# Optimization experiments

Measured on AMD Instinct MI355X. Metric: run time of the kernel, lower is better.

## Reference

```python
import jax, jax.numpy as jnp
import numpy as np

D_MODEL = 1024
N_INPUT = 4096
N_PROCESS = 2048
D_ROUTING = 256
TEMPERATURE = 0.5
LN_EPS = 1e-5


def _gelu(x):
    return jax.nn.gelu(x, approximate=False)  # torch F.gelu default (erf)


def setup_inputs() -> dict:
    key = jax.random.key(0)
    ks = jax.random.split(key, 10)
    B, S = 8, 2048
    x = jax.random.normal(ks[0], (B, S, D_MODEL), dtype=jnp.float32)
    # GlobalRouter query_net: Linear(d_model, 2*d_routing) -> GELU -> LayerNorm -> Linear(2*d_routing, d_routing)
    W1 = jax.random.normal(ks[1], (2 * D_ROUTING, D_MODEL), dtype=jnp.float32) * (2.0 / (D_MODEL + 2 * D_ROUTING)) ** 0.5 * 1.414
    b1 = jnp.zeros((2 * D_ROUTING,), dtype=jnp.float32)
    ln_g = jnp.ones((2 * D_ROUTING,), dtype=jnp.float32)
    ln_b = jnp.zeros((2 * D_ROUTING,), dtype=jnp.float32)
    W2 = jax.random.normal(ks[2], (D_ROUTING, 2 * D_ROUTING), dtype=jnp.float32) * (2.0 / (3 * D_ROUTING)) ** 0.5 * 1.414
    b2 = jnp.zeros((D_ROUTING,), dtype=jnp.float32)
    neuron_keys = jax.random.normal(ks[3], (N_INPUT, D_ROUTING), dtype=jnp.float32) / D_ROUTING ** 0.5 * 1.414
    input_patterns = jax.random.normal(ks[4], (N_INPUT, D_MODEL), dtype=jnp.float32) / D_MODEL ** 0.5 * 1.414
    process_weights = jax.random.normal(ks[5], (N_PROCESS, N_INPUT), dtype=jnp.float32) / N_INPUT ** 0.5 * 1.414
    process_outputs = jax.random.normal(ks[6], (N_PROCESS, D_MODEL), dtype=jnp.float32) / D_MODEL ** 0.5 * 1.414
    return {
        'x': x, 'k_input': 2048, 'k_process': 1024,
        'W1': W1, 'b1': b1, 'ln_g': ln_g, 'ln_b': ln_b, 'W2': W2, 'b2': b2,
        'neuron_keys': neuron_keys, 'input_patterns': input_patterns,
        'process_weights': process_weights, 'process_outputs': process_outputs,
    }


def _forward(x, k_input, k_process, W1, b1, ln_g, ln_b, W2, b2,
             neuron_keys, input_patterns, process_weights, process_outputs):
    B, S, d_model = x.shape
    # ---- GlobalRouter ----
    gctx = jnp.max(x, axis=1)                                  # [B, d_model]
    h = _gelu(gctx @ W1.T + b1)                                # [B, 2*d_routing]
    mu = jnp.mean(h, axis=-1, keepdims=True)
    var = jnp.mean((h - mu) ** 2, axis=-1, keepdims=True)
    h = (h - mu) * jax.lax.rsqrt(var + LN_EPS) * ln_g + ln_b
    query = h @ W2.T + b2                                      # [B, d_routing]
    logits = (query @ neuron_keys.T) / D_ROUTING ** 0.5        # [B, n_input]
    probs = jax.nn.softmax(logits / TEMPERATURE, axis=-1)
    _, input_idx = jax.lax.top_k(logits, k_input)              # [B, k_input]
    one_hot = jnp.zeros_like(probs).at[jnp.arange(B)[:, None], input_idx].set(1.0)
    routing_weights = jax.lax.stop_gradient(one_hot - probs) + probs  # STE
    # ---- input neuron stage ----
    input_acts = _gelu(jnp.einsum('bsd,nd->bsn', x, input_patterns))   # [B,S,n_input]
    weighted = input_acts * routing_weights[:, None, :]
    sel_in = jnp.take_along_axis(weighted, input_idx[:, None, :], axis=2)  # [B,S,k_input]
    # gather process weight columns per batch: [B, n_process, k_input]
    W_sel = jnp.transpose(process_weights[:, input_idx], (1, 0, 2))
    process_acts = _gelu(jnp.einsum('bsk,bpk->bsp', sel_in, W_sel))    # [B,S,n_process]
    # ---- process neuron stage ----
    process_scores = jnp.mean(process_acts, axis=1)                    # [B,n_process]
    _, process_idx = jax.lax.top_k(process_scores, k_process)          # [B,k_process]
    sel_proc = jnp.take_along_axis(process_acts, process_idx[:, None, :], axis=2)  # [B,S,k_process]
    out_sel = process_outputs[process_idx]                             # [B,k_process,d_model]
    return jnp.einsum('bsp,bpd->bsd', sel_proc, out_sel)


def reference(x, k_input, k_process, W1, b1, ln_g, ln_b, W2, b2,
              neuron_keys, input_patterns, process_weights, process_outputs):
    return _forward(x, k_input, k_process, W1, b1, ln_g, ln_b, W2, b2,
                    neuron_keys, input_patterns, process_weights, process_outputs)
```

## Files before the change

kernel.cpp:

```cpp
#include <hip/hip_runtime.h>
#include <stdint.h>

#define B_  8
#define S_  2048
#define DM  1024
#define NI  4096
#define NP  2048
#define DR  256
#define H2  512
#define KI  2048
#define KP  1024
#define LDW 40

typedef __attribute__((ext_vector_type(8))) short bf16x8;
typedef __attribute__((ext_vector_type(4))) float f32x4;
typedef unsigned short ushort;
typedef unsigned int uint;

__device__ __forceinline__ float gelu_erf(float v){
    return 0.5f * v * (1.0f + erff(v * 0.7071067811865476f));
}
__device__ __forceinline__ ushort f2b(float f){
    union { float f; uint u; } a; a.f = f;
    uint r = a.u + 0x7fffu + ((a.u >> 16) & 1u);
    return (ushort)(r >> 16);
}
__device__ __forceinline__ float b2f(ushort u){
    union { uint u; float f; } a; a.u = ((uint)u) << 16; return a.f;
}
__device__ __forceinline__ void cvt8(const float* p, uint4& H, uint4& L){
    uint h[4], l[4];
    #pragma unroll
    for(int i = 0; i < 4; i++){
        ushort h0 = f2b(p[2*i]);   float f0 = b2f(h0); ushort l0 = f2b(p[2*i]   - f0);
        ushort h1 = f2b(p[2*i+1]); float f1 = b2f(h1); ushort l1 = f2b(p[2*i+1] - f1);
        h[i] = (uint)h0 | ((uint)h1 << 16);
        l[i] = (uint)l0 | ((uint)l1 << 16);
    }
    H = uint4{h[0],h[1],h[2],h[3]};
    L = uint4{l[0],l[1],l[2],l[3]};
}
__device__ __forceinline__ void gload_lds16(const void* g, void* l){
    __builtin_amdgcn_global_load_lds((const __attribute__((address_space(1))) void*)g,
                                     (__attribute__((address_space(3))) void*)l, 16, 0, 0);
}

__global__ __launch_bounds__(256) void k_cvt(const float* __restrict__ src,
                                             ushort* __restrict__ hi,
                                             ushort* __restrict__ lo){
    size_t idx = (size_t)blockIdx.x*256 + threadIdx.x;
    float f[8];
    *(float4*)(f)     = ((const float4*)src)[idx*2];
    *(float4*)(f + 4) = ((const float4*)src)[idx*2 + 1];
    uint4 H, L; cvt8(f, H, L);
    ((uint4*)hi)[idx] = H;
    ((uint4*)lo)[idx] = L;
}

__global__ __launch_bounds__(256) void k_gpart(const float* __restrict__ x,
                                               float* __restrict__ gpart){
    int b = blockIdx.x >> 4, ch = blockIdx.x & 15;
    const float4* xb = (const float4*)(x + ((size_t)b*S_ + (size_t)ch*128) * DM);
    int t = threadIdx.x;
    float4 m = xb[t];
    for(int r = 1; r < 128; r++){
        float4 v = xb[(size_t)r*(DM/4) + t];
        m.x = fmaxf(m.x, v.x); m.y = fmaxf(m.y, v.y);
        m.z = fmaxf(m.z, v.z); m.w = fmaxf(m.w, v.w);
    }
    ((float4*)(gpart + (size_t)(b*16 + ch)*DM))[t] = m;
}

__global__ __launch_bounds__(256) void k_h(const float* __restrict__ gpart,
                                           const float* __restrict__ W1,
                                           const float* __restrict__ b1,
                                           float* __restrict__ h){
    __shared__ float g[DM];
    int b = blockIdx.x >> 3, ig = blockIdx.x & 7;
    int t = threadIdx.x;
    for(int d = t; d < DM; d += 256){
        float m = gpart[(size_t)(b*16)*DM + d];
        for(int c = 1; c < 16; c++) m = fmaxf(m, gpart[(size_t)(b*16 + c)*DM + d]);
        g[d] = m;
    }
    __syncthreads();
    int i  = ig*64 + (t >> 2);
    int dq = (t & 3) * 256;
    const float* wr = W1 + (size_t)i*DM + dq;
    const float* gg = g + dq;
    float s = 0.f;
    for(int d = 0; d < 256; d++) s = fmaf(gg[d], wr[d], s);
    s += __shfl_xor(s, 1);
    s += __shfl_xor(s, 2);
    if((t & 3) == 0) h[b*H2 + i] = gelu_erf(s + b1[i]);
}

__global__ __launch_bounds__(256) void k_query(const float* __restrict__ h,
                                               const float* __restrict__ lng,
                                               const float* __restrict__ lnb,
                                               const float* __restrict__ W2,
                                               const float* __restrict__ b2,
                                               float* __restrict__ query){
    __shared__ float hn[H2];
    __shared__ float red[4];
    int b = blockIdx.x >> 2, qg = blockIdx.x & 3;
    int t = threadIdx.x;
    float v0 = h[b*H2 + t], v1 = h[b*H2 + 256 + t];
    float s = v0 + v1;
    for(int o = 32; o > 0; o >>= 1) s += __shfl_down(s, o);
    if((t & 63) == 0) red[t >> 6] = s;
    __syncthreads();
    float mean = (red[0] + red[1] + red[2] + red[3]) * (1.f/H2);
    __syncthreads();
    float d0 = v0 - mean, d1 = v1 - mean;
    float sq = d0*d0 + d1*d1;
    for(int o = 32; o > 0; o >>= 1) sq += __shfl_down(sq, o);
    if((t & 63) == 0) red[t >> 6] = sq;
    __syncthreads();
    float var  = (red[0] + red[1] + red[2] + red[3]) * (1.f/H2);
    float rstd = rsqrtf(var + 1e-5f);
    hn[t]       = d0*rstd*lng[t]       + lnb[t];
    hn[256 + t] = d1*rstd*lng[256 + t] + lnb[256 + t];
    __syncthreads();
    int q  = qg*64 + (t >> 2);
    int iq = (t & 3) * 128;
    const float* wr = W2 + (size_t)q*H2 + iq;
    float acc = 0.f;
    for(int i2 = 0; i2 < 128; i2++) acc = fmaf(hn[iq + i2], wr[i2], acc);
    acc += __shfl_xor(acc, 1);
    acc += __shfl_xor(acc, 2);
    if((t & 3) == 0) query[b*DR + q] = acc + b2[q];
}

__global__ __launch_bounds__(256) void k_logits(const float* __restrict__ query,
                                                const float* __restrict__ nk,
                                                float* __restrict__ logits){
    __shared__ float q[DR];
    int b = blockIdx.x >> 4, ng = blockIdx.x & 15;
    int t = threadIdx.x;
    if(t < DR) q[t] = query[b*DR + t];
    __syncthreads();
    int n = ng*256 + t;
    const float* kr = nk + (size_t)n*DR;
    float s = 0.f;
    for(int i = 0; i < DR; i++) s = fmaf(q[i], kr[i], s);
    logits[b*NI + n] = s * 0.0625f;
}

template<int N_, int KSEL>
__global__ __launch_bounds__(256) void k_topk(const float* __restrict__ vals,
                                              int* __restrict__ idxout){
    __shared__ unsigned u[N_];
    __shared__ int redc[4];
    __shared__ int sc[256];
    int t = threadIdx.x;
    size_t vbase = (size_t)blockIdx.x * N_;
    size_t obase = (size_t)blockIdx.x * KSEL;
    for(int i = t; i < N_; i += 256){
        unsigned bits = __float_as_uint(vals[vbase + i]);
        u[i] = (bits & 0x80000000u) ? ~bits : (bits | 0x80000000u);
    }
    __syncthreads();
    unsigned lo = 0u, hi = 0xFFFFFFFFu;
    while(lo < hi){
        unsigned mid = lo + (unsigned)((((unsigned long long)(hi - lo)) + 1ull) >> 1);
        int c = 0;
        for(int i = t; i < N_; i += 256) c += (u[i] >= mid) ? 1 : 0;
        for(int o = 32; o > 0; o >>= 1) c += __shfl_down(c, o);
        if((t & 63) == 0) redc[t >> 6] = c;
        __syncthreads();
        int tot = redc[0] + redc[1] + redc[2] + redc[3];
        if(tot >= KSEL) lo = mid; else hi = mid - 1;
        __syncthreads();
    }
    unsigned T = lo;
    const int PER = N_ / 256;
    int base = t * PER;
    int lgt = 0, leq = 0;
    for(int j = 0; j < PER; j++){
        unsigned v = u[base + j];
        lgt += (v > T) ? 1 : 0; leq += (v == T) ? 1 : 0;
    }
    sc[t] = (lgt << 16) | leq;
    __syncthreads();
    for(int o = 1; o < 256; o <<= 1){
        int add = (t >= o) ? sc[t - o] : 0;
        __syncthreads();
        sc[t] += add;
        __syncthreads();
    }
    int need = KSEL - (sc[255] >> 16);
    int ex = (t == 0) ? 0 : sc[t - 1];
    int pos = (ex >> 16) + ((ex & 0xffff) < need ? (ex & 0xffff) : need);
    int eq = ex & 0xffff;
    for(int j = 0; j < PER; j++){
        unsigned v = u[base + j];
        if(v > T){ idxout[obase + pos++] = base + j; }
        else if(v == T){ if(eq < need){ idxout[obase + pos++] = base + j; } eq++; }
    }
}

__global__ __launch_bounds__(256) void k_gemm1(const ushort* __restrict__ xh,
                                               const ushort* __restrict__ xl,
                                               const ushort* __restrict__ ph,
                                               const ushort* __restrict__ pl,
                                               const int* __restrict__ iidx,
                                               ushort* __restrict__ selh,
                                               ushort* __restrict__ sell, int b0){
    __shared__ __align__(16) ushort Ah[2][128*32], Al[2][128*32], Bh[2][128*32], Bl[2][128*32];
    __shared__ int rowmap[128];
    int t = threadIdx.x;
    int g = blockIdx.x >> 8, rest = blockIdx.x & 255;
    int b = b0 + g;
    int mb = rest >> 4, nb = rest & 15;
    int m0 = mb*128, n0 = nb*128;
    ushort* selh_g = selh + (size_t)g*S_*KI;
    ushort* sell_g = sell + (size_t)g*S_*KI;
    if(t < 128) rowmap[t] = iidx[(size_t)b*KI + n0 + t];
    __syncthreads();
    int w = t >> 6, l = t & 63;
    int lr = l >> 2, lc = l & 3;
    int r0 = 32*w + lr, r1 = r0 + 16;
    const ushort* pAh0 = xh + ((size_t)b*S_ + m0 + r0)*DM + lc*8;
    const ushort* pAh1 = xh + ((size_t)b*S_ + m0 + r1)*DM + lc*8;
    const ushort* pAl0 = xl + ((size_t)b*S_ + m0 + r0)*DM + lc*8;
    const ushort* pAl1 = xl + ((size_t)b*S_ + m0 + r1)*DM + lc*8;
    const ushort* pBh0 = ph + (size_t)rowmap[r0]*DM + lc*8;
    const ushort* pBh1 = ph + (size_t)rowmap[r1]*DM + lc*8;
    const ushort* pBl0 = pl + (size_t)rowmap[r0]*DM + lc*8;
    const ushort* pBl1 = pl + (size_t)rowmap[r1]*DM + lc*8;
    int d0 = w*1024, d1 = d0 + 512;
    #define STG1(BUF, KO) do{ \
        gload_lds16(pAh0 + (KO), &Ah[BUF][d0]); \
        gload_lds16(pAh1 + (KO), &Ah[BUF][d1]); \
        gload_lds16(pAl0 + (KO), &Al[BUF][d0]); \
        gload_lds16(pAl1 + (KO), &Al[BUF][d1]); \
        gload_lds16(pBh0 + (KO), &Bh[BUF][d0]); \
        gload_lds16(pBh1 + (KO), &Bh[BUF][d1]); \
        gload_lds16(pBl0 + (KO), &Bl[BUF][d0]); \
        gload_lds16(pBl1 + (KO), &Bl[BUF][d1]); \
    }while(0)
    STG1(0, 0);
    int lm = l & 15, q = l >> 4;
    int mbase = (w >> 1)*64, nbase = (w & 1)*64;
    f32x4 acc[4][4];
    #pragma unroll
    for(int i = 0; i < 4; i++)
      #pragma unroll
      for(int j = 0; j < 4; j++) acc[i][j] = f32x4{0.f,0.f,0.f,0.f};
    int cur = 0;
    for(int k0 = 0; k0 < DM; k0 += 32){
        if(k0 + 32 < DM){
            STG1(cur^1, k0 + 32);
            asm volatile("s_waitcnt vmcnt(8)" ::: "memory");
        }else{
            asm volatile("s_waitcnt vmcnt(0)" ::: "memory");
        }
        __builtin_amdgcn_s_barrier();
        asm volatile("" ::: "memory");
        bf16x8 ahf[4], alf[4];
        #pragma unroll
        for(int mt = 0; mt < 4; mt++){
            ahf[mt] = *(const bf16x8*)(&Ah[cur][(mbase + mt*16 + lm)*32 + q*8]);
            alf[mt] = *(const bf16x8*)(&Al[cur][(mbase + mt*16 + lm)*32 + q*8]);
        }
        __builtin_amdgcn_s_setprio(1);
        #pragma unroll
        for(int nt = 0; nt < 4; nt++){
            bf16x8 bhf = *(const bf16x8*)(&Bh[cur][(nbase + nt*16 + lm)*32 + q*8]);
            bf16x8 blf = *(const bf16x8*)(&Bl[cur][(nbase + nt*16 + lm)*32 + q*8]);
            #pragma unroll
            for(int mt = 0; mt < 4; mt++){
                acc[mt][nt] = __builtin_amdgcn_mfma_f32_16x16x32_bf16(ahf[mt], bhf, acc[mt][nt], 0, 0, 0);
                acc[mt][nt] = __builtin_amdgcn_mfma_f32_16x16x32_bf16(ahf[mt], blf, acc[mt][nt], 0, 0, 0);
                acc[mt][nt] = __builtin_amdgcn_mfma_f32_16x16x32_bf16(alf[mt], bhf, acc[mt][nt], 0, 0, 0);
            }
        }
        __builtin_amdgcn_s_setprio(0);
        asm volatile("s_waitcnt lgkmcnt(0)" ::: "memory");
        __builtin_amdgcn_s_barrier();
        asm volatile("" ::: "memory");
        cur ^= 1;
    }
    #undef STG1
    #pragma unroll
    for(int mt = 0; mt < 4; mt++)
      #pragma unroll
      for(int nt = 0; nt < 4; nt++){
        int col = n0 + nbase + nt*16 + lm;
        #pragma unroll
        for(int i = 0; i < 4; i++){
            int row = m0 + mbase + mt*16 + q*4 + i;
            float gv = gelu_erf(acc[mt][nt][i]);
            ushort hbits = f2b(gv);
            selh_g[(size_t)row*KI + col] = hbits;
            sell_g[(size_t)row*KI + col] = f2b(gv - b2f(hbits));
        }
      }
}

__global__ __launch_bounds__(256) void k_gather_wsel(const float* __restrict__ pw,
                                                     const int* __restrict__ iidx,
                                                     ushort* __restrict__ wh,
                                                     ushort* __restrict__ wl,
                                                     float* __restrict__ scores, int b0){
    __shared__ int kidx[KI];
    int g = blockIdx.x >> 8, pc = blockIdx.x & 255;
    int b = b0 + g;
    ushort* wh_g = wh + (size_t)g*NP*KI;
    ushort* wl_g = wl + (size_t)g*NP*KI;
    int t = threadIdx.x;
    for(int i = t; i < KI; i += 256) kidx[i] = iidx[(size_t)b*KI + i];
    if(t < 8) scores[(size_t)b*NP + pc*8 + t] = 0.f;
    __syncthreads();
    for(int r2 = 0; r2 < 8; r2++){
        int p = pc*8 + r2;
        const float* row = pw + (size_t)p*NI;
        for(int j = t; j < KI; j += 256){
            float v = row[kidx[j]];
            ushort hb = f2b(v);
            wh_g[(size_t)p*KI + j] = hb;
            wl_g[(size_t)p*KI + j] = f2b(v - b2f(hb));
        }
    }
}

__global__ __launch_bounds__(256) void k_gemm2(const ushort* __restrict__ selh,
                                               const ushort* __restrict__ sell,
                                               const ushort* __restrict__ wh,
                                               const ushort* __restrict__ wl,
                                               ushort* __restrict__ acts,
                                               float* __restrict__ scores, int b0){
    __shared__ __align__(16) ushort Ah[2][128*32], Al[2][128*32], Bh[2][128*32], Bl[2][128*32];
    __shared__ float colsum[128];
    int t = threadIdx.x;
    int g = blockIdx.x >> 8, rest = blockIdx.x & 255;
    int b = b0 + g;
    int mb = rest >> 4, nb = rest & 15;
    int m0 = mb*128, n0 = nb*128;
    const ushort* selh_g = selh + (size_t)g*S_*KI;
    const ushort* sell_g = sell + (size_t)g*S_*KI;
    const ushort* wh_g   = wh   + (size_t)g*NP*KI;
    const ushort* wl_g   = wl   + (size_t)g*NP*KI;
    ushort* acts_g = acts + (size_t)g*S_*NP;
    int w = t >> 6, l = t & 63;
    int lr = l >> 2, lc = l & 3;
    int r0 = 32*w + lr, r1 = r0 + 16;
    const ushort* pAh0 = selh_g + (size_t)(m0 + r0)*KI + lc*8;
    const ushort* pAh1 = selh_g + (size_t)(m0 + r1)*KI + lc*8;
    const ushort* pAl0 = sell_g + (size_t)(m0 + r0)*KI + lc*8;
    const ushort* pAl1 = sell_g + (size_t)(m0 + r1)*KI + lc*8;
    const ushort* pBh0 = wh_g + (size_t)(n0 + r0)*KI + lc*8;
    const ushort* pBh1 = wh_g + (size_t)(n0 + r1)*KI + lc*8;
    const ushort* pBl0 = wl_g + (size_t)(n0 + r0)*KI + lc*8;
    const ushort* pBl1 = wl_g + (size_t)(n0 + r1)*KI + lc*8;
    int d0 = w*1024, d1 = d0 + 512;
    #define STG2(BUF, KO) do{ \
        gload_lds16(pAh0 + (KO), &Ah[BUF][d0]); \
        gload_lds16(pAh1 + (KO), &Ah[BUF][d1]); \
        gload_lds16(pAl0 + (KO), &Al[BUF][d0]); \
        gload_lds16(pAl1 + (KO), &Al[BUF][d1]); \
        gload_lds16(pBh0 + (KO), &Bh[BUF][d0]); \
        gload_lds16(pBh1 + (KO), &Bh[BUF][d1]); \
        gload_lds16(pBl0 + (KO), &Bl[BUF][d0]); \
        gload_lds16(pBl1 + (KO), &Bl[BUF][d1]); \
    }while(0)
    STG2(0, 0);
    int lm = l & 15, q = l >> 4;
    int mbase = (w >> 1)*64, nbase = (w & 1)*64;
    f32x4 acc[4][4];
    #pragma unroll
    for(int i = 0; i < 4; i++)
      #pragma unroll
      for(int j = 0; j < 4; j++) acc[i][j] = f32x4{0.f,0.f,0.f,0.f};
    int cur = 0;
    for(int k0 = 0; k0 < KI; k0 += 32){
        if(k0 + 32 < KI){
            STG2(cur^1, k0 + 32);
            asm volatile("s_waitcnt vmcnt(8)" ::: "memory");
        }else{
            asm volatile("s_waitcnt vmcnt(0)" ::: "memory");
        }
        __builtin_amdgcn_s_barrier();
        asm volatile("" ::: "memory");
        bf16x8 ahf[4], alf[4];
        #pragma unroll
        for(int mt = 0; mt < 4; mt++){
            ahf[mt] = *(const bf16x8*)(&Ah[cur][(mbase + mt*16 + lm)*32 + q*8]);
            alf[mt] = *(const bf16x8*)(&Al[cur][(mbase + mt*16 + lm)*32 + q*8]);
        }
        __builtin_amdgcn_s_setprio(1);
        #pragma unroll
        for(int nt = 0; nt < 4; nt++){
            bf16x8 bhf = *(const bf16x8*)(&Bh[cur][(nbase + nt*16 + lm)*32 + q*8]);
            bf16x8 blf = *(const bf16x8*)(&Bl[cur][(nbase + nt*16 + lm)*32 + q*8]);
            #pragma unroll
            for(int mt = 0; mt < 4; mt++){
                acc[mt][nt] = __builtin_amdgcn_mfma_f32_16x16x32_bf16(ahf[mt], bhf, acc[mt][nt], 0, 0, 0);
                acc[mt][nt] = __builtin_amdgcn_mfma_f32_16x16x32_bf16(ahf[mt], blf, acc[mt][nt], 0, 0, 0);
                acc[mt][nt] = __builtin_amdgcn_mfma_f32_16x16x32_bf16(alf[mt], bhf, acc[mt][nt], 0, 0, 0);
            }
        }
        __builtin_amdgcn_s_setprio(0);
        asm volatile("s_waitcnt lgkmcnt(0)" ::: "memory");
        __builtin_amdgcn_s_barrier();
        asm volatile("" ::: "memory");
        cur ^= 1;
    }
    #undef STG2
    if(t < 128) colsum[t] = 0.f;
    __syncthreads();
    #pragma unroll
    for(int mt = 0; mt < 4; mt++)
      #pragma unroll
      for(int nt = 0; nt < 4; nt++){
        int cb = nbase + nt*16 + lm;
        float s4 = 0.f;
        #pragma unroll
        for(int i = 0; i < 4; i++){
            int row = m0 + mbase + mt*16 + q*4 + i;
            float gv = gelu_erf(acc[mt][nt][i]);
            s4 += gv;
            acts_g[(size_t)row*NP + n0 + cb] = f2b(gv);
        }
        atomicAdd(&colsum[cb], s4);
      }
    __syncthreads();
    if(t < 128) atomicAdd(&scores[(size_t)b*NP + n0 + t], colsum[t]);
}

__global__ __launch_bounds__(256) void k_gather_selacts(const ushort* __restrict__ acts,
                                                        const int* __restrict__ pidx,
                                                        ushort* __restrict__ selacts, int b0){
    __shared__ int pix[KP];
    int g = blockIdx.x >> 6, sc_ = blockIdx.x & 63;
    int b = b0 + g;
    const ushort* acts_g = acts + (size_t)g*S_*NP;
    ushort* selacts_g = selacts + (size_t)g*S_*KP;
    int t = threadIdx.x;
    for(int i = t; i < KP; i += 256) pix[i] = pidx[(size_t)b*KP + i];
    __syncthreads();
    const ushort* Ab = acts_g    + ((size_t)sc_*32)*NP;
    ushort*       Ob = selacts_g + ((size_t)sc_*32)*KP;
    for(int r2 = 0; r2 < 32; r2++){
        for(int j = t; j < KP; j += 256)
            Ob[(size_t)r2*KP + j] = Ab[(size_t)r2*NP + pix[j]];
    }
}

__global__ __launch_bounds__(256) void k_gemm3(const ushort* __restrict__ selacts,
                                               const float* __restrict__ pout,
                                               const int* __restrict__ pidx,
                                               float* __restrict__ out, int b0){
    __shared__ __align__(16) ushort As[128*LDW], Bs[128*LDW];
    __shared__ int pix[KP];
    int t = threadIdx.x;
    int g = blockIdx.x >> 7, rest = blockIdx.x & 127;
    int b = b0 + g;
    int mb = rest >> 3, nb = rest & 7;
    int m0 = mb*128, n0 = nb*128;
    const ushort* selacts_g = selacts + (size_t)g*S_*KP;
    for(int i = t; i < KP; i += 256) pix[i] = pidx[(size_t)b*KP + i];
    __syncthreads();
    int r = t & 127, half = t >> 7;
    const ushort* ag = selacts_g + (size_t)(m0 + r)*KP + half*16;
    int kk = t >> 3, nc = (t & 7)*16;
    uint4 A0 = *(const uint4*)(ag), A1 = *(const uint4*)(ag + 8);
    float4 fb[4];
    {
        const float* bg = pout + (size_t)pix[kk]*DM + n0 + nc;
        #pragma unroll
        for(int i = 0; i < 4; i++) fb[i] = *(const float4*)(bg + i*4);
    }
    int w = t >> 6, lane = t & 63;
    int mbase = (w >> 1)*64, nbase = (w & 1)*64;
    int lm = lane & 15, q = lane >> 4;
    f32x4 acc[4][4];
    #pragma unroll
    for(int i = 0; i < 4; i++)
      #pragma unroll
      for(int j = 0; j < 4; j++) acc[i][j] = f32x4{0.f,0.f,0.f,0.f};
    for(int k0 = 0; k0 < KP; k0 += 32){
        __syncthreads();
        *(uint4*)(As + r*LDW + half*16)     = A0;
        *(uint4*)(As + r*LDW + half*16 + 8) = A1;
        {
            const float* pf = (const float*)fb;
            #pragma unroll
            for(int c = 0; c < 16; c++) Bs[(nc + c)*LDW + kk] = f2b(pf[c]);
        }
        __syncthreads();
        if(k0 + 32 < KP){
            ag += 32;
            A0 = *(const uint4*)(ag); A1 = *(const uint4*)(ag + 8);
            const float* bg = pout + (size_t)pix[k0 + 32 + kk]*DM + n0 + nc;
            #pragma unroll
            for(int i = 0; i < 4; i++) fb[i] = *(const float4*)(bg + i*4);
        }
        bf16x8 af[4];
        #pragma unroll
        for(int mt = 0; mt < 4; mt++)
            af[mt] = *(const bf16x8*)(As + (mbase + mt*16 + lm)*LDW + q*8);
        #pragma unroll
        for(int nt = 0; nt < 4; nt++){
            bf16x8 bf = *(const bf16x8*)(Bs + (nbase + nt*16 + lm)*LDW + q*8);
            #pragma unroll
            for(int mt = 0; mt < 4; mt++)
                acc[mt][nt] = __builtin_amdgcn_mfma_f32_16x16x32_bf16(af[mt], bf, acc[mt][nt], 0, 0, 0);
        }
    }
    float* Cb = out + (size_t)b*S_*DM;
    #pragma unroll
    for(int mt = 0; mt < 4; mt++)
      #pragma unroll
      for(int nt = 0; nt < 4; nt++){
        int col = n0 + nbase + nt*16 + lm;
        #pragma unroll
        for(int i = 0; i < 4; i++){
            int row = m0 + mbase + mt*16 + q*4 + i;
            Cb[(size_t)row*DM + col] = acc[mt][nt][i];
        }
      }
}

extern "C" void kernel_launch(void* const* d_in, const int* in_sizes, int n_in,
                              void* d_out, int out_size, void* d_ws, size_t ws_size,
                              hipStream_t stream){
    const float* x    = (const float*)d_in[0];
    const float* W1   = (const float*)d_in[3];
    const float* b1   = (const float*)d_in[4];
    const float* lng  = (const float*)d_in[5];
    const float* lnb  = (const float*)d_in[6];
    const float* W2   = (const float*)d_in[7];
    const float* b2   = (const float*)d_in[8];
    const float* nk   = (const float*)d_in[9];
    const float* patt = (const float*)d_in[10];
    const float* pw   = (const float*)d_in[11];
    const float* pout = (const float*)d_in[12];
    float* out = (float*)d_out;

    auto al256 = [](size_t v){ return (v + 255) & ~(size_t)255; };
    const size_t fixed =
        al256((size_t)B_*16*DM*4) + al256((size_t)B_*H2*4) + al256((size_t)B_*DR*4) +
        al256((size_t)B_*NI*4)    + al256((size_t)B_*KI*4) + al256((size_t)B_*NP*4) +
        al256((size_t)B_*KP*4) +
        2*al256((size_t)B_*S_*DM*2) + 2*al256((size_t)NI*DM*2);
    const size_t perb = (size_t)S_*KI*2*2 + (size_t)NP*KI*2*2 + (size_t)S_*NP*2 + (size_t)S_*KP*2 + 6*256;
    int G = 4;
    while(G > 1 && fixed + (size_t)G*perb > ws_size) G >>= 1;
    if(fixed + (size_t)G*perb > ws_size) return;

    char* wsp = (char*)d_ws;
    size_t off = 0;
    auto alloc = [&](size_t bytes) -> void* {
        void* p = wsp + off;
        off += (bytes + 255) & ~(size_t)255;
        return p;
    };
    float*  gpart   = (float*) alloc((size_t)B_*16*DM*4);
    float*  h       = (float*) alloc((size_t)B_*H2*4);
    float*  query   = (float*) alloc((size_t)B_*DR*4);
    float*  logits  = (float*) alloc((size_t)B_*NI*4);
    int*    iidx    = (int*)   alloc((size_t)B_*KI*4);
    float*  scores  = (float*) alloc((size_t)B_*NP*4);
    int*    pidx    = (int*)   alloc((size_t)B_*KP*4);
    ushort* xh      = (ushort*)alloc((size_t)B_*S_*DM*2);
    ushort* xl      = (ushort*)alloc((size_t)B_*S_*DM*2);
    ushort* patth   = (ushort*)alloc((size_t)NI*DM*2);
    ushort* pattl   = (ushort*)alloc((size_t)NI*DM*2);
    ushort* selh    = (ushort*)alloc((size_t)G*S_*KI*2);
    ushort* sell    = (ushort*)alloc((size_t)G*S_*KI*2);
    ushort* wselh   = (ushort*)alloc((size_t)G*NP*KI*2);
    ushort* wsell   = (ushort*)alloc((size_t)G*NP*KI*2);
    ushort* acts    = (ushort*)alloc((size_t)G*S_*NP*2);
    ushort* selacts = (ushort*)alloc((size_t)G*S_*KP*2);

    dim3 blk(256);
    k_cvt   <<<(B_*S_*DM/8)/256, blk, 0, stream>>>(x, xh, xl);
    k_cvt   <<<(NI*DM/8)/256,    blk, 0, stream>>>(patt, patth, pattl);
    k_gpart <<<128, blk, 0, stream>>>(x, gpart);
    k_h     <<<64,  blk, 0, stream>>>(gpart, W1, b1, h);
    k_query <<<32,  blk, 0, stream>>>(h, lng, lnb, W2, b2, query);
    k_logits<<<128, blk, 0, stream>>>(query, nk, logits);
    k_topk<NI, KI><<<B_, blk, 0, stream>>>(logits, iidx);
    for(int b0 = 0; b0 < B_; b0 += G){
        k_gemm1        <<<G*256, blk, 0, stream>>>(xh, xl, patth, pattl, iidx, selh, sell, b0);
        k_gather_wsel  <<<G*256, blk, 0, stream>>>(pw, iidx, wselh, wsell, scores, b0);
        k_gemm2        <<<G*256, blk, 0, stream>>>(selh, sell, wselh, wsell, acts, scores, b0);
        k_topk<NP, KP> <<<G,     blk, 0, stream>>>(scores + (size_t)b0*NP, pidx + (size_t)b0*KP);
        k_gather_selacts<<<G*64, blk, 0, stream>>>(acts, pidx, selacts, b0);
        k_gemm3        <<<G*128, blk, 0, stream>>>(selacts, pout, pidx, out, b0);
    }
}
```

Baseline: 1.465 ms.

## Fuse max-pool with x conversion, vectorize gathers, pipeline gemm3 with bf16 outputs

The global max over x is now computed in the same pass that converts x to bf16 hi/lo halves, so x is read once instead of twice. process_outputs is converted to bf16 once up front, and gemm3 double-buffers its A tile through direct global-to-LDS loads with explicit waitcnt and barriers. The index gathers in gather_wsel and gather_selacts read their indices straight into registers and issue vectorized stores. The default batch group size rises from 4 to 8 when workspace allows, cutting the number of loop iterations and launches. The cost is more workspace and hand-written synchronization in gemm3.

```diff
diff --git a/kernel.cpp b/kernel.cpp
--- a/kernel.cpp
+++ b/kernel.cpp
@@ -45,6 +45,29 @@
                                      (__attribute__((address_space(3))) void*)l, 16, 0, 0);
 }
 
+__global__ __launch_bounds__(256) void k_gpart_cvt(const float* __restrict__ x,
+                                                   float* __restrict__ gpart,
+                                                   ushort* __restrict__ xh,
+                                                   ushort* __restrict__ xl){
+    int b = blockIdx.x >> 5, ch = blockIdx.x & 31;
+    size_t row0 = (size_t)b*S_ + (size_t)ch*64;
+    const float4* xb = (const float4*)(x + row0*DM);
+    int t = threadIdx.x;
+    float4 m = float4{-3.402823466e38f, -3.402823466e38f, -3.402823466e38f, -3.402823466e38f};
+    for(int r = 0; r < 64; r++){
+        float4 v = xb[(size_t)r*(DM/4) + t];
+        ushort hx = f2b(v.x), hy = f2b(v.y), hz = f2b(v.z), hw = f2b(v.w);
+        uint2 H{ (uint)hx | ((uint)hy << 16), (uint)hz | ((uint)hw << 16) };
+        uint2 L{ (uint)f2b(v.x - b2f(hx)) | ((uint)f2b(v.y - b2f(hy)) << 16),
+                 (uint)f2b(v.z - b2f(hz)) | ((uint)f2b(v.w - b2f(hw)) << 16) };
+        ((uint2*)(xh + (row0 + r)*DM))[t] = H;
+        ((uint2*)(xl + (row0 + r)*DM))[t] = L;
+        m.x = fmaxf(m.x, v.x); m.y = fmaxf(m.y, v.y);
+        m.z = fmaxf(m.z, v.z); m.w = fmaxf(m.w, v.w);
+    }
+    ((float4*)(gpart + (size_t)(b*32 + ch)*DM))[t] = m;
+}
+
 __global__ __launch_bounds__(256) void k_cvt(const float* __restrict__ src,
                                              ushort* __restrict__ hi,
                                              ushort* __restrict__ lo){
@@ -57,18 +80,17 @@
     ((uint4*)lo)[idx] = L;
 }
 
-__global__ __launch_bounds__(256) void k_gpart(const float* __restrict__ x,
-                                               float* __restrict__ gpart){
-    int b = blockIdx.x >> 4, ch = blockIdx.x & 15;
-    const float4* xb = (const float4*)(x + ((size_t)b*S_ + (size_t)ch*128) * DM);
-    int t = threadIdx.x;
-    float4 m = xb[t];
-    for(int r = 1; r < 128; r++){
-        float4 v = xb[(size_t)r*(DM/4) + t];
-        m.x = fmaxf(m.x, v.x); m.y = fmaxf(m.y, v.y);
-        m.z = fmaxf(m.z, v.z); m.w = fmaxf(m.w, v.w);
-    }
-    ((float4*)(gpart + (size_t)(b*16 + ch)*DM))[t] = m;
+__global__ __launch_bounds__(256) void k_cvt1(const float* __restrict__ src,
+                                              ushort* __restrict__ dst){
+    size_t idx = (size_t)blockIdx.x*256 + threadIdx.x;
+    float f[8];
+    *(float4*)(f)     = ((const float4*)src)[idx*2];
+    *(float4*)(f + 4) = ((const float4*)src)[idx*2 + 1];
+    uint o[4];
+    #pragma unroll
+    for(int i = 0; i < 4; i++)
+        o[i] = (uint)f2b(f[2*i]) | ((uint)f2b(f[2*i+1]) << 16);
+    ((uint4*)dst)[idx] = uint4{o[0], o[1], o[2], o[3]};
 }
 
 __global__ __launch_bounds__(256) void k_h(const float* __restrict__ gpart,
@@ -79,8 +101,8 @@
     int b = blockIdx.x >> 3, ig = blockIdx.x & 7;
     int t = threadIdx.x;
     for(int d = t; d < DM; d += 256){
-        float m = gpart[(size_t)(b*16)*DM + d];
-        for(int c = 1; c < 16; c++) m = fmaxf(m, gpart[(size_t)(b*16 + c)*DM + d]);
+        float m = gpart[(size_t)(b*32)*DM + d];
+        for(int c = 1; c < 32; c++) m = fmaxf(m, gpart[(size_t)(b*32 + c)*DM + d]);
         g[d] = m;
     }
     __syncthreads();
@@ -304,24 +326,29 @@
                                                      ushort* __restrict__ wh,
                                                      ushort* __restrict__ wl,
                                                      float* __restrict__ scores, int b0){
-    __shared__ int kidx[KI];
     int g = blockIdx.x >> 8, pc = blockIdx.x & 255;
     int b = b0 + g;
     ushort* wh_g = wh + (size_t)g*NP*KI;
     ushort* wl_g = wl + (size_t)g*NP*KI;
     int t = threadIdx.x;
-    for(int i = t; i < KI; i += 256) kidx[i] = iidx[(size_t)b*KI + i];
     if(t < 8) scores[(size_t)b*NP + pc*8 + t] = 0.f;
-    __syncthreads();
+    int j0 = t*8;
+    int k8[8];
+    *(int4*)(k8)     = *(const int4*)(iidx + (size_t)b*KI + j0);
+    *(int4*)(k8 + 4) = *(const int4*)(iidx + (size_t)b*KI + j0 + 4);
     for(int r2 = 0; r2 < 8; r2++){
         int p = pc*8 + r2;
         const float* row = pw + (size_t)p*NI;
-        for(int j = t; j < KI; j += 256){
-            float v = row[kidx[j]];
-            ushort hb = f2b(v);
-            wh_g[(size_t)p*KI + j] = hb;
-            wl_g[(size_t)p*KI + j] = f2b(v - b2f(hb));
-        }
+        uint hh[4], ll[4];
+        #pragma unroll
+        for(int i = 0; i < 4; i++){
+            float v0 = row[k8[2*i]], v1 = row[k8[2*i+1]];
+            ushort h0 = f2b(v0), h1 = f2b(v1);
+            hh[i] = (uint)h0 | ((uint)h1 << 16);
+            ll[i] = (uint)f2b(v0 - b2f(h0)) | ((uint)f2b(v1 - b2f(h1)) << 16);
+        }
+        *(uint4*)(wh_g + (size_t)p*KI + j0) = uint4{hh[0],hh[1],hh[2],hh[3]};
+        *(uint4*)(wl_g + (size_t)p*KI + j0) = uint4{ll[0],ll[1],ll[2],ll[3]};
     }
 }
 
@@ -432,82 +459,99 @@
 __global__ __launch_bounds__(256) void k_gather_selacts(const ushort* __restrict__ acts,
                                                         const int* __restrict__ pidx,
                                                         ushort* __restrict__ selacts, int b0){
-    __shared__ int pix[KP];
     int g = blockIdx.x >> 6, sc_ = blockIdx.x & 63;
     int b = b0 + g;
     const ushort* acts_g = acts + (size_t)g*S_*NP;
     ushort* selacts_g = selacts + (size_t)g*S_*KP;
     int t = threadIdx.x;
-    for(int i = t; i < KP; i += 256) pix[i] = pidx[(size_t)b*KP + i];
-    __syncthreads();
+    int j0 = t*4;
+    int4 p4 = *(const int4*)(pidx + (size_t)b*KP + j0);
     const ushort* Ab = acts_g    + ((size_t)sc_*32)*NP;
     ushort*       Ob = selacts_g + ((size_t)sc_*32)*KP;
     for(int r2 = 0; r2 < 32; r2++){
-        for(int j = t; j < KP; j += 256)
-            Ob[(size_t)r2*KP + j] = Ab[(size_t)r2*NP + pix[j]];
+        const ushort* Ar = Ab + (size_t)r2*NP;
+        ushort o0 = Ar[p4.x], o1 = Ar[p4.y], o2 = Ar[p4.z], o3 = Ar[p4.w];
+        uint2 ov{ (uint)o0 | ((uint)o1 << 16), (uint)o2 | ((uint)o3 << 16) };
+        *(uint2*)(Ob + (size_t)r2*KP + j0) = ov;
     }
 }
 
 __global__ __launch_bounds__(256) void k_gemm3(const ushort* __restrict__ selacts,
-                                               const float* __restrict__ pout,
+                                               const ushort* __restrict__ poutb,
                                                const int* __restrict__ pidx,
                                                float* __restrict__ out, int b0){
-    __shared__ __align__(16) ushort As[128*LDW], Bs[128*LDW];
+    __shared__ __align__(16) ushort As[2][128*32];
+    __shared__ __align__(16) ushort Bs[2][128*LDW];
     __shared__ int pix[KP];
     int t = threadIdx.x;
     int g = blockIdx.x >> 7, rest = blockIdx.x & 127;
     int b = b0 + g;
     int mb = rest >> 3, nb = rest & 7;
     int m0 = mb*128, n0 = nb*128;
-    const ushort* selacts_g = selacts + (size_t)g*S_*KP;
+    const ushort* sel_g = selacts + (size_t)g*S_*KP;
+    int w = t >> 6, l = t & 63;
+    int lr = l >> 2, lc = l & 3;
+    int r0 = 32*w + lr, r1 = r0 + 16;
+    const ushort* pA0 = sel_g + (size_t)(m0 + r0)*KP + lc*8;
+    const ushort* pA1 = sel_g + (size_t)(m0 + r1)*KP + lc*8;
+    int d0 = w*1024, d1 = d0 + 512;
+    gload_lds16(pA0, &As[0][d0]);
+    gload_lds16(pA1, &As[0][d1]);
     for(int i = t; i < KP; i += 256) pix[i] = pidx[(size_t)b*KP + i];
     __syncthreads();
-    int r = t & 127, half = t >> 7;
-    const ushort* ag = selacts_g + (size_t)(m0 + r)*KP + half*16;
     int kk = t >> 3, nc = (t & 7)*16;
-    uint4 A0 = *(const uint4*)(ag), A1 = *(const uint4*)(ag + 8);
-    float4 fb[4];
+    uint4 B0, B1;
     {
-        const float* bg = pout + (size_t)pix[kk]*DM + n0 + nc;
-        #pragma unroll
-        for(int i = 0; i < 4; i++) fb[i] = *(const float4*)(bg + i*4);
-    }
-    int w = t >> 6, lane = t & 63;
+        const ushort* bg = poutb + (size_t)pix[kk]*DM + n0 + nc;
+        B0 = *(const uint4*)(bg); B1 = *(const uint4*)(bg + 8);
+    }
+    int lm = l & 15, q = l >> 4;
     int mbase = (w >> 1)*64, nbase = (w & 1)*64;
-    int lm = lane & 15, q = lane >> 4;
     f32x4 acc[4][4];
     #pragma unroll
     for(int i = 0; i < 4; i++)
       #pragma unroll
       for(int j = 0; j < 4; j++) acc[i][j] = f32x4{0.f,0.f,0.f,0.f};
     for(int k0 = 0; k0 < KP; k0 += 32){
-        __syncthreads();
-        *(uint4*)(As + r*LDW + half*16)     = A0;
-        *(uint4*)(As + r*LDW + half*16 + 8) = A1;
+        int cur = (k0 >> 5) & 1;
         {
-            const float* pf = (const float*)fb;
+            const ushort* pb0 = (const ushort*)&B0;
+            const ushort* pb1 = (const ushort*)&B1;
             #pragma unroll
-            for(int c = 0; c < 16; c++) Bs[(nc + c)*LDW + kk] = f2b(pf[c]);
-        }
-        __syncthreads();
+            for(int c = 0; c < 8; c++) Bs[cur][(nc + c)*LDW + kk]     = pb0[c];
+            #pragma unroll
+            for(int c = 0; c < 8; c++) Bs[cur][(nc + 8 + c)*LDW + kk] = pb1[c];
+        }
         if(k0 + 32 < KP){
-            ag += 32;
-            A0 = *(const uint4*)(ag); A1 = *(const uint4*)(ag + 8);
-            const float* bg = pout + (size_t)pix[k0 + 32 + kk]*DM + n0 + nc;
-            #pragma unroll
-            for(int i = 0; i < 4; i++) fb[i] = *(const float4*)(bg + i*4);
+            gload_lds16(pA0 + (k0 + 32), &As[cur^1][d0]);
+            gload_lds16(pA1 + (k0 + 32), &As[cur^1][d1]);
+            asm volatile("s_waitcnt vmcnt(2)" ::: "memory");
+        }else{
+            asm volatile("s_waitcnt vmcnt(0)" ::: "memory");
+        }
+        asm volatile("s_waitcnt lgkmcnt(0)" ::: "memory");
+        __builtin_amdgcn_s_barrier();
+        asm volatile("" ::: "memory");
+        if(k0 + 32 < KP){
+            const ushort* bg = poutb + (size_t)pix[k0 + 32 + kk]*DM + n0 + nc;
+            B0 = *(const uint4*)(bg); B1 = *(const uint4*)(bg + 8);
         }
         bf16x8 af[4];
         #pragma unroll
         for(int mt = 0; mt < 4; mt++)
-            af[mt] = *(const bf16x8*)(As + (mbase + mt*16 + lm)*LDW + q*8);
+            af[mt] = *(const bf16x8*)(&As[cur][(mbase + mt*16 + lm)*32 + q*8]);
+        __builtin_amdgcn_s_setprio(1);
         #pragma unroll
         for(int nt = 0; nt < 4; nt++){
-            bf16x8 bf = *(const bf16x8*)(Bs + (nbase + nt*16 + lm)*LDW + q*8);
+            bf16x8 bf = *(const bf16x8*)(&Bs[cur][(nbase + nt*16 + lm)*LDW + q*8]);
             #pragma unroll
             for(int mt = 0; mt < 4; mt++)
                 acc[mt][nt] = __builtin_amdgcn_mfma_f32_16x16x32_bf16(af[mt], bf, acc[mt][nt], 0, 0, 0);
         }
+        __builtin_amdgcn_s_setprio(0);
+        asm volatile("s_waitcnt lgkmcnt(0)" ::: "memory");
+        __builtin_amdgcn_s_barrier();
+        asm volatile("" ::: "memory");
     }
     float* Cb = out + (size_t)b*S_*DM;
     #pragma unroll
@@ -541,12 +585,12 @@
 
     auto al256 = [](size_t v){ return (v + 255) & ~(size_t)255; };
     const size_t fixed =
-        al256((size_t)B_*16*DM*4) + al256((size_t)B_*H2*4) + al256((size_t)B_*DR*4) +
+        al256((size_t)B_*32*DM*4) + al256((size_t)B_*H2*4) + al256((size_t)B_*DR*4) +
         al256((size_t)B_*NI*4)    + al256((size_t)B_*KI*4) + al256((size_t)B_*NP*4) +
         al256((size_t)B_*KP*4) +
-        2*al256((size_t)B_*S_*DM*2) + 2*al256((size_t)NI*DM*2);
+        2*al256((size_t)B_*S_*DM*2) + 2*al256((size_t)NI*DM*2) + al256((size_t)NP*DM*2);
     const size_t perb = (size_t)S_*KI*2*2 + (size_t)NP*KI*2*2 + (size_t)S_*NP*2 + (size_t)S_*KP*2 + 6*256;
-    int G = 4;
+    int G = 8;
     while(G > 1 && fixed + (size_t)G*perb > ws_size) G >>= 1;
     if(fixed + (size_t)G*perb > ws_size) return;
 
@@ -557,7 +601,7 @@
         off += (bytes + 255) & ~(size_t)255;
         return p;
     };
-    float*  gpart   = (float*) alloc((size_t)B_*16*DM*4);
+    float*  gpart   = (float*) alloc((size_t)B_*32*DM*4);
     float*  h       = (float*) alloc((size_t)B_*H2*4);
     float*  query   = (float*) alloc((size_t)B_*DR*4);
     float*  logits  = (float*) alloc((size_t)B_*NI*4);
@@ -568,6 +612,7 @@
     ushort* xl      = (ushort*)alloc((size_t)B_*S_*DM*2);
     ushort* patth   = (ushort*)alloc((size_t)NI*DM*2);
     ushort* pattl   = (ushort*)alloc((size_t)NI*DM*2);
+    ushort* poutb   = (ushort*)alloc((size_t)NP*DM*2);
     ushort* selh    = (ushort*)alloc((size_t)G*S_*KI*2);
     ushort* sell    = (ushort*)alloc((size_t)G*S_*KI*2);
     ushort* wselh   = (ushort*)alloc((size_t)G*NP*KI*2);
@@ -576,9 +621,9 @@
     ushort* selacts = (ushort*)alloc((size_t)G*S_*KP*2);
 
     dim3 blk(256);
-    k_cvt   <<<(B_*S_*DM/8)/256, blk, 0, stream>>>(x, xh, xl);
-    k_cvt   <<<(NI*DM/8)/256,    blk, 0, stream>>>(patt, patth, pattl);
-    k_gpart <<<128, blk, 0, stream>>>(x, gpart);
+    k_gpart_cvt<<<B_*32, blk, 0, stream>>>(x, gpart, xh, xl);
+    k_cvt   <<<(NI*DM/8)/256, blk, 0, stream>>>(patt, patth, pattl);
+    k_cvt1  <<<(NP*DM/8)/256, blk, 0, stream>>>(pout, poutb);
     k_h     <<<64,  blk, 0, stream>>>(gpart, W1, b1, h);
     k_query <<<32,  blk, 0, stream>>>(h, lng, lnb, W2, b2, query);
     k_logits<<<128, blk, 0, stream>>>(query, nk, logits);
@@ -589,6 +634,6 @@
         k_gemm2        <<<G*256, blk, 0, stream>>>(selh, sell, wselh, wsell, acts, scores, b0);
         k_topk<NP, KP> <<<G,     blk, 0, stream>>>(scores + (size_t)b0*NP, pidx + (size_t)b0*KP);
         k_gather_selacts<<<G*64, blk, 0, stream>>>(acts, pidx, selacts, b0);
-        k_gemm3        <<<G*128, blk, 0, stream>>>(selacts, pout, pidx, out, b0);
-    }
-}
+        k_gemm3        <<<G*128, blk, 0, stream>>>(selacts, poutb, pidx, out, b0);
+    }
+}
```

After: 1.297 ms. -11.5%, faster.
